# Kernel tuning notes

Hardware: AMD Instinct MI355X
Metric: run time of the kernel (lower is better)

## Reference

```python
import jax, jax.numpy as jnp
import numpy as np

B = 1_000_000  # number of tracklets
STATE_DIM, OBS_DIM = 6, 3


def setup_inputs() -> dict:
    key = jax.random.key(0)
    k1, k2, k3, k4 = jax.random.split(key, 4)
    x = jax.random.normal(k1, (B, STATE_DIM, 1), dtype=jnp.float32)
    # P: symmetric PSD covariance, eye + small random A A^T
    A = 0.1 * jax.random.normal(k2, (B, STATE_DIM, STATE_DIM), dtype=jnp.float32)
    P = jnp.einsum('bij,bkj->bik', A, A) + jnp.eye(STATE_DIM, dtype=jnp.float32)
    delta_t = jax.random.uniform(k3, (B,), dtype=jnp.float32, minval=0.01, maxval=0.2)
    Q = jnp.broadcast_to(0.01 * jnp.eye(STATE_DIM, dtype=jnp.float32), (B, STATE_DIM, STATE_DIM))
    z = jax.random.normal(k4, (B, OBS_DIM, 1), dtype=jnp.float32)
    R = jnp.broadcast_to(0.1 * jnp.eye(OBS_DIM, dtype=jnp.float32), (B, OBS_DIM, OBS_DIM))
    return {"x": x, "P": P, "delta_t": delta_t, "Q": Q, "z": z, "R": R}


def reference(x, P, delta_t, Q, z, R):
    """One batched EKF step: predict(delta_t, Q) then update(z, R).
    Returns (x_upd [B,6,1], P_upd [B,6,6])."""
    Bn = x.shape[0]
    dt = delta_t.reshape(-1)
    # F = I6 with dt on the (pos, vel) off-diagonal entries (0,3),(1,4),(2,5)
    shift = jnp.zeros((STATE_DIM, STATE_DIM), x.dtype).at[
        jnp.array([0, 1, 2]), jnp.array([3, 4, 5])].set(1.0)
    F = jnp.eye(STATE_DIM, dtype=x.dtype) + dt[:, None, None] * shift  # [B,6,6]

    # Predict
    x_pred = F @ x                                           # [B,6,1]
    P_pred = F @ P @ jnp.swapaxes(F, -1, -2) + Q             # [B,6,6]

    # Update (H selects first 3 state rows, so H@P == P[:, :3, :], etc.)
    S = P_pred[:, :OBS_DIM, :OBS_DIM] + R                    # [B,3,3]
    K = P_pred[:, :, :OBS_DIM] @ jnp.linalg.inv(S)           # [B,6,3]
    innov = z - x_pred[:, :OBS_DIM, :]                       # [B,3,1]
    x_upd = x_pred + K @ innov                               # [B,6,1]
    # K @ H places K in the first 3 columns of a [B,6,6] matrix
    KH = jnp.concatenate([K, jnp.zeros((Bn, STATE_DIM, STATE_DIM - OBS_DIM), x.dtype)], axis=2)
    P_upd = P_pred - KH @ P_pred                             # (I - K H) P
    return x_upd, P_upd
```

## Files before the change

### kernel.cpp

```cpp
#include <hip/hip_runtime.h>


#define BLK 256

__global__ __launch_bounds__(BLK, 5)
void ekf_step_r7(const float* __restrict__ x_in,
                 const float* __restrict__ P_in,
                 const float* __restrict__ dt_in,
                 const float* __restrict__ Q_in,
                 const float* __restrict__ z_in,
                 const float* __restrict__ R_in,
                 float* __restrict__ x_out,
                 float* __restrict__ P_out,
                 int B)
{
    const int t = blockIdx.x * BLK + threadIdx.x;
    if (t >= B) return;

    float Qu[36];
#pragma unroll
    for (int j = 0; j < 36; ++j) Qu[j] = Q_in[j];
    float Ru[9];
#pragma unroll
    for (int j = 0; j < 9; ++j) Ru[j] = R_in[j];

    float P[36];
    {
        const float4* pr = (const float4*)(P_in + (size_t)t * 36);
#pragma unroll
        for (int k = 0; k < 9; ++k) {
            float4 v = pr[k];
            P[k*4+0] = v.x; P[k*4+1] = v.y; P[k*4+2] = v.z; P[k*4+3] = v.w;
        }
    }

    const float dt = dt_in[t];

    float x[6];
    {
        const float2* p = (const float2*)(x_in + (size_t)t * 6);
        float2 a = p[0], b = p[1], c = p[2];
        x[0]=a.x; x[1]=a.y; x[2]=b.x; x[3]=b.y; x[4]=c.x; x[5]=c.y;
    }
    float zv[3];
    {
        const float* p = z_in + (size_t)t * 3;
        zv[0]=p[0]; zv[1]=p[1]; zv[2]=p[2];
    }

    float xp[6];
#pragma unroll
    for (int i = 0; i < 3; ++i) xp[i] = fmaf(dt, x[i+3], x[i]);
    xp[3]=x[3]; xp[4]=x[4]; xp[5]=x[5];

#pragma unroll
    for (int i = 0; i < 3; ++i)
#pragma unroll
        for (int j = 0; j < 6; ++j)
            P[i*6+j] = fmaf(dt, P[(i+3)*6+j], P[i*6+j]);
#pragma unroll
    for (int i = 0; i < 6; ++i)
#pragma unroll
        for (int j = 0; j < 3; ++j)
            P[i*6+j] = fmaf(dt, P[i*6+j+3], P[i*6+j]);
#pragma unroll
    for (int j = 0; j < 36; ++j)
        P[j] += Qu[j];

    const float S00 = P[0]  + Ru[0], S01 = P[1]  + Ru[1], S02 = P[2]  + Ru[2];
    const float S10 = P[6]  + Ru[3], S11 = P[7]  + Ru[4], S12 = P[8]  + Ru[5];
    const float S20 = P[12] + Ru[6], S21 = P[13] + Ru[7], S22 = P[14] + Ru[8];

    const float c00 =  (S11*S22 - S12*S21);
    const float c01 = -(S10*S22 - S12*S20);
    const float c02 =  (S10*S21 - S11*S20);
    const float c10 = -(S01*S22 - S02*S21);
    const float c11 =  (S00*S22 - S02*S20);
    const float c12 = -(S00*S21 - S01*S20);
    const float c20 =  (S01*S12 - S02*S11);
    const float c21 = -(S00*S12 - S02*S10);
    const float c22 =  (S00*S11 - S01*S10);
    const float det  = S00*c00 + S01*c01 + S02*c02;
    const float rdet = 1.0f / det;

    float Si[9];
    Si[0]=c00*rdet; Si[1]=c10*rdet; Si[2]=c20*rdet;
    Si[3]=c01*rdet; Si[4]=c11*rdet; Si[5]=c21*rdet;
    Si[6]=c02*rdet; Si[7]=c12*rdet; Si[8]=c22*rdet;

    float K[18];
#pragma unroll
    for (int i = 0; i < 6; ++i)
#pragma unroll
        for (int a = 0; a < 3; ++a)
            K[i*3+a] = P[i*6+0]*Si[0*3+a] + P[i*6+1]*Si[1*3+a] + P[i*6+2]*Si[2*3+a];

    const float iv0 = zv[0] - xp[0];
    const float iv1 = zv[1] - xp[1];
    const float iv2 = zv[2] - xp[2];

    float xu[6];
#pragma unroll
    for (int i = 0; i < 6; ++i)
        xu[i] = xp[i] + K[i*3+0]*iv0 + K[i*3+1]*iv1 + K[i*3+2]*iv2;

    {
        float2* p = (float2*)(x_out + (size_t)t * 6);
        p[0] = make_float2(xu[0], xu[1]);
        p[1] = make_float2(xu[2], xu[3]);
        p[2] = make_float2(xu[4], xu[5]);
    }

    float T[18];
#pragma unroll
    for (int j = 0; j < 18; ++j) T[j] = P[j];
#pragma unroll
    for (int i = 0; i < 6; ++i)
#pragma unroll
        for (int j = 0; j < 6; ++j)
            P[i*6+j] -= K[i*3+0]*T[j] + K[i*3+1]*T[6+j] + K[i*3+2]*T[12+j];

    {
        float4* gq = (float4*)(P_out + (size_t)t * 36);
#pragma unroll
        for (int k = 0; k < 9; ++k)
            gq[k] = make_float4(P[k*4+0], P[k*4+1], P[k*4+2], P[k*4+3]);
    }
}

extern "C" void kernel_launch(void* const* d_in, const int* in_sizes, int n_in,
                              void* d_out, int out_size, void* d_ws, size_t ws_size,
                              hipStream_t stream) {
    const float* x_in  = (const float*)d_in[0];
    const float* P_in  = (const float*)d_in[1];
    const float* dt_in = (const float*)d_in[2];
    const float* Q_in  = (const float*)d_in[3];
    const float* z_in  = (const float*)d_in[4];
    const float* R_in  = (const float*)d_in[5];

    const int B = in_sizes[2];

    float* x_out = (float*)d_out;
    float* P_out = (float*)d_out + (size_t)B * 6;

    const int grid = (B + BLK - 1) / BLK;
    ekf_step_r7<<<grid, BLK, 0, stream>>>(x_in, P_in, dt_in, Q_in, z_in, R_in,
                                          x_out, P_out, B);
}
```

Before: 382.9 us.

## Use persistent grid-stride loop with double-buffered register prefetch and nontemporal stores

Replaces the one-thread-per-tracklet launch with a capped grid of 1024 blocks that loops over tracklets. Each thread prefetches the next tracklet's P, x, z and dt into a second register buffer while it computes the current one, so memory latency overlaps with math. Outputs are written with nontemporal stores, and the occupancy hint drops from 5 to 4 blocks per SIMD. The second buffer raises register pressure and cuts occupancy, and the capped grid may leave the memory pipes less saturated than a full launch would.

Measured after the change: 668.4 us. +74.6%, slower.

```diff
diff --git a/kernel.cpp b/kernel.cpp
--- a/kernel.cpp
+++ b/kernel.cpp
@@ -2,56 +2,65 @@
 
 
 #define BLK 256
-
-__global__ __launch_bounds__(BLK, 5)
-void ekf_step_r7(const float* __restrict__ x_in,
-                 const float* __restrict__ P_in,
-                 const float* __restrict__ dt_in,
-                 const float* __restrict__ Q_in,
-                 const float* __restrict__ z_in,
-                 const float* __restrict__ R_in,
-                 float* __restrict__ x_out,
-                 float* __restrict__ P_out,
-                 int B)
+#define MAXG 1024
+
+typedef float vf4 __attribute__((ext_vector_type(4)));
+typedef float vf2 __attribute__((ext_vector_type(2)));
+
+struct Trk {
+    vf4   pv[9];
+    float x0,x1,x2,x3,x4,x5;
+    float z0,z1,z2;
+    float dt;
+};
+
+__device__ __forceinline__ void load_trk(Trk& T, int t, int B,
+                                         const float* __restrict__ P_in,
+                                         const float* __restrict__ x_in,
+                                         const float* __restrict__ z_in,
+                                         const float* __restrict__ dt_in)
 {
-    const int t = blockIdx.x * BLK + threadIdx.x;
-    if (t >= B) return;
-
-    float Qu[36];
-#pragma unroll
-    for (int j = 0; j < 36; ++j) Qu[j] = Q_in[j];
-    float Ru[9];
-#pragma unroll
-    for (int j = 0; j < 9; ++j) Ru[j] = R_in[j];
+    const bool v = (t < B);
+    const vf4* pr = (const vf4*)(P_in + (size_t)t * 36);
+#pragma unroll
+    for (int k = 0; k < 9; ++k) {
+        T.pv[k] = (vf4)(0.f);
+        if (v) T.pv[k] = pr[k];
+    }
+    T.x0=T.x1=T.x2=T.x3=T.x4=T.x5=0.f;
+    if (v) {
+        const vf2* p = (const vf2*)(x_in + (size_t)t * 6);
+        vf2 a = p[0], b = p[1], c = p[2];
+        T.x0=a.x; T.x1=a.y; T.x2=b.x; T.x3=b.y; T.x4=c.x; T.x5=c.y;
+    }
+    T.z0=T.z1=T.z2=0.f;
+    if (v) {
+        const float* p = z_in + (size_t)t * 3;
+        T.z0=p[0]; T.z1=p[1]; T.z2=p[2];
+    }
+    T.dt = 0.f;
+    if (v) T.dt = dt_in[t];
+}
+
+__device__ __forceinline__ void proc_trk(const Trk& T, int t, int B,
+                                         const float* Qu, const float* Ru,
+                                         float* __restrict__ x_out,
+                                         float* __restrict__ P_out)
+{
+    const float dt = T.dt;
 
     float P[36];
-    {
-        const float4* pr = (const float4*)(P_in + (size_t)t * 36);
-#pragma unroll
-        for (int k = 0; k < 9; ++k) {
-            float4 v = pr[k];
-            P[k*4+0] = v.x; P[k*4+1] = v.y; P[k*4+2] = v.z; P[k*4+3] = v.w;
-        }
-    }
-
-    const float dt = dt_in[t];
-
-    float x[6];
-    {
-        const float2* p = (const float2*)(x_in + (size_t)t * 6);
-        float2 a = p[0], b = p[1], c = p[2];
-        x[0]=a.x; x[1]=a.y; x[2]=b.x; x[3]=b.y; x[4]=c.x; x[5]=c.y;
-    }
-    float zv[3];
-    {
-        const float* p = z_in + (size_t)t * 3;
-        zv[0]=p[0]; zv[1]=p[1]; zv[2]=p[2];
+#pragma unroll
+    for (int k = 0; k < 9; ++k) {
+        P[k*4+0]=T.pv[k].x; P[k*4+1]=T.pv[k].y;
+        P[k*4+2]=T.pv[k].z; P[k*4+3]=T.pv[k].w;
     }
 
     float xp[6];
-#pragma unroll
-    for (int i = 0; i < 3; ++i) xp[i] = fmaf(dt, x[i+3], x[i]);
-    xp[3]=x[3]; xp[4]=x[4]; xp[5]=x[5];
+    xp[0] = fmaf(dt, T.x3, T.x0);
+    xp[1] = fmaf(dt, T.x4, T.x1);
+    xp[2] = fmaf(dt, T.x5, T.x2);
+    xp[3] = T.x3; xp[4] = T.x4; xp[5] = T.x5;
 
 #pragma unroll
     for (int i = 0; i < 3; ++i)
@@ -95,36 +104,78 @@
         for (int a = 0; a < 3; ++a)
             K[i*3+a] = P[i*6+0]*Si[0*3+a] + P[i*6+1]*Si[1*3+a] + P[i*6+2]*Si[2*3+a];
 
-    const float iv0 = zv[0] - xp[0];
-    const float iv1 = zv[1] - xp[1];
-    const float iv2 = zv[2] - xp[2];
-
-    float xu[6];
-#pragma unroll
-    for (int i = 0; i < 6; ++i)
-        xu[i] = xp[i] + K[i*3+0]*iv0 + K[i*3+1]*iv1 + K[i*3+2]*iv2;
-
-    {
-        float2* p = (float2*)(x_out + (size_t)t * 6);
-        p[0] = make_float2(xu[0], xu[1]);
-        p[1] = make_float2(xu[2], xu[3]);
-        p[2] = make_float2(xu[4], xu[5]);
-    }
-
-    float T[18];
-#pragma unroll
-    for (int j = 0; j < 18; ++j) T[j] = P[j];
-#pragma unroll
-    for (int i = 0; i < 6; ++i)
-#pragma unroll
-        for (int j = 0; j < 6; ++j)
-            P[i*6+j] -= K[i*3+0]*T[j] + K[i*3+1]*T[6+j] + K[i*3+2]*T[12+j];
-
-    {
-        float4* gq = (float4*)(P_out + (size_t)t * 36);
-#pragma unroll
-        for (int k = 0; k < 9; ++k)
-            gq[k] = make_float4(P[k*4+0], P[k*4+1], P[k*4+2], P[k*4+3]);
+    const float iv0 = T.z0 - xp[0];
+    const float iv1 = T.z1 - xp[1];
+    const float iv2 = T.z2 - xp[2];
+
+    const bool v = (t < B);
+    if (v) {
+        vf2* p = (vf2*)(x_out + (size_t)t * 6);
+        vf2 r0 = {xp[0] + K[0]*iv0  + K[1]*iv1  + K[2]*iv2,
+                  xp[1] + K[3]*iv0  + K[4]*iv1  + K[5]*iv2};
+        vf2 r1 = {xp[2] + K[6]*iv0  + K[7]*iv1  + K[8]*iv2,
+                  xp[3] + K[9]*iv0  + K[10]*iv1 + K[11]*iv2};
+        vf2 r2 = {xp[4] + K[12]*iv0 + K[13]*iv1 + K[14]*iv2,
+                  xp[5] + K[15]*iv0 + K[16]*iv1 + K[17]*iv2};
+        __builtin_nontemporal_store(r0, p + 0);
+        __builtin_nontemporal_store(r1, p + 1);
+        __builtin_nontemporal_store(r2, p + 2);
+    }
+
+#pragma unroll
+    for (int j = 0; j < 6; ++j) {
+        const float p0 = P[j], p1 = P[6+j], p2 = P[12+j];
+#pragma unroll
+        for (int i = 0; i < 6; ++i)
+            P[i*6+j] -= K[i*3+0]*p0 + K[i*3+1]*p1 + K[i*3+2]*p2;
+    }
+
+    if (v) {
+        vf4* gq = (vf4*)(P_out + (size_t)t * 36);
+#pragma unroll
+        for (int k = 0; k < 9; ++k) {
+            vf4 w = {P[k*4+0], P[k*4+1], P[k*4+2], P[k*4+3]};
+            __builtin_nontemporal_store(w, gq + k);
+        }
+    }
+}
+
+__global__ __launch_bounds__(BLK, 4)
+void ekf_step_r10(const float* __restrict__ x_in,
+                  const float* __restrict__ P_in,
+                  const float* __restrict__ dt_in,
+                  const float* __restrict__ Q_in,
+                  const float* __restrict__ z_in,
+                  const float* __restrict__ R_in,
+                  float* __restrict__ x_out,
+                  float* __restrict__ P_out,
+                  int B)
+{
+    const int tid0   = blockIdx.x * BLK + threadIdx.x;
+    const int stride = gridDim.x * BLK;
+    const int niter  = (B + stride - 1) / stride;
+
+    float Qu[36];
+#pragma unroll
+    for (int j = 0; j < 36; ++j) Qu[j] = Q_in[j];
+    float Ru[9];
+#pragma unroll
+    for (int j = 0; j < 9; ++j) Ru[j] = R_in[j];
+
+    Trk A, Bb;
+    load_trk(A, tid0, B, P_in, x_in, z_in, dt_in);
+
+    int k = 0;
+    while (true) {
+        if (k + 1 < niter)
+            load_trk(Bb, tid0 + (k+1)*stride, B, P_in, x_in, z_in, dt_in);
+        proc_trk(A, tid0 + k*stride, B, Qu, Ru, x_out, P_out);
+        ++k; if (k == niter) break;
+
+        if (k + 1 < niter)
+            load_trk(A, tid0 + (k+1)*stride, B, P_in, x_in, z_in, dt_in);
+        proc_trk(Bb, tid0 + k*stride, B, Qu, Ru, x_out, P_out);
+        ++k; if (k == niter) break;
     }
 }
 
@@ -143,7 +194,8 @@
     float* x_out = (float*)d_out;
     float* P_out = (float*)d_out + (size_t)B * 6;
 
-    const int grid = (B + BLK - 1) / BLK;
-    ekf_step_r7<<<grid, BLK, 0, stream>>>(x_in, P_in, dt_in, Q_in, z_in, R_in,
-                                          x_out, P_out, B);
-}
+    int grid = (B + BLK - 1) / BLK;
+    if (grid > MAXG) grid = MAXG;
+    ekf_step_r10<<<grid, BLK, 0, stream>>>(x_in, P_in, dt_in, Q_in, z_in, R_in,
+                                           x_out, P_out, B);
+}
```

## Stage inputs through LDS with async global_load_lds triple-buffered persistent pipeline

Applied to the files above, without the earlier changes.

Replaces the one-thread-per-tracklet kernel with a persistent grid of 64-thread blocks. Each block walks 64-element tiles and stages P, x, z and dt into a three-slot LDS ring using direct global-to-LDS loads, overlapping the loads for later tiles with compute on the current one through vmcnt waits. Outputs use nontemporal stores. This aims to get coalesced, deeply pipelined memory traffic for a bandwidth-bound kernel, but the grid is capped at 1024 blocks of 64 threads, which limits occupancy and depends on hand-counted vmcnt values being correct.

After: 652.4 us. 70.4% more time.

```diff
diff --git a/kernel.cpp b/kernel.cpp
--- a/kernel.cpp
+++ b/kernel.cpp
@@ -1,57 +1,92 @@
 #include <hip/hip_runtime.h>
 
 
-#define BLK 256
-
-__global__ __launch_bounds__(BLK, 5)
-void ekf_step_r7(const float* __restrict__ x_in,
-                 const float* __restrict__ P_in,
-                 const float* __restrict__ dt_in,
-                 const float* __restrict__ Q_in,
-                 const float* __restrict__ z_in,
-                 const float* __restrict__ R_in,
-                 float* __restrict__ x_out,
-                 float* __restrict__ P_out,
-                 int B)
+#define BLK   64
+#define TFL   2944
+#define XOFF  2304
+#define ZOFF  2688
+#define DOFF  2880
+#define MAXG  1024
+
+typedef float vf4 __attribute__((ext_vector_type(4)));
+typedef float vf2 __attribute__((ext_vector_type(2)));
+
+__device__ __forceinline__ void gl16(const float* g, float* l) {
+    __builtin_amdgcn_global_load_lds(
+        (const __attribute__((address_space(1))) void*)g,
+        (__attribute__((address_space(3))) void*)l, 16, 0, 0);
+}
+__device__ __forceinline__ void gl4(const float* g, float* l) {
+    __builtin_amdgcn_global_load_lds(
+        (const __attribute__((address_space(1))) void*)g,
+        (__attribute__((address_space(3))) void*)l, 4, 0, 0);
+}
+
+#define VMWAIT(N) do { \
+    asm volatile("s_waitcnt vmcnt(" #N ")" ::: "memory"); \
+    __builtin_amdgcn_sched_barrier(0); \
+} while (0)
+
+__device__ __forceinline__ void stage_tile(float* buf, int tt, int lane,
+    const float* __restrict__ P_in, const float* __restrict__ x_in,
+    const float* __restrict__ z_in, const float* __restrict__ dt_in,
+    int pmax, int xmax, int zmax, int dmax)
 {
-    const int t = blockIdx.x * BLK + threadIdx.x;
-    if (t >= B) return;
-
-    float Qu[36];
-#pragma unroll
-    for (int j = 0; j < 36; ++j) Qu[j] = Q_in[j];
-    float Ru[9];
-#pragma unroll
-    for (int j = 0; j < 9; ++j) Ru[j] = R_in[j];
+#pragma unroll
+    for (int op = 0; op < 9; ++op) {
+        int e = tt*2304 + op*256 + lane*4;
+        e = min(e, pmax);
+        gl16(P_in + e, buf + op*256);
+    }
+#pragma unroll
+    for (int op = 0; op < 6; ++op) {
+        int e = tt*384 + op*64 + lane;
+        e = min(e, xmax);
+        gl4(x_in + e, buf + XOFF + op*64);
+    }
+#pragma unroll
+    for (int op = 0; op < 3; ++op) {
+        int e = tt*192 + op*64 + lane;
+        e = min(e, zmax);
+        gl4(z_in + e, buf + ZOFF + op*64);
+    }
+    {
+        int e = tt*64 + lane;
+        e = min(e, dmax);
+        gl4(dt_in + e, buf + DOFF);
+    }
+}
+
+__device__ __forceinline__ void proc_tile(const float* buf, int tt, int lane,
+    int B, const float* Qu, const float* Ru,
+    float* __restrict__ x_out, float* __restrict__ P_out)
+{
+    const int t = tt*64 + lane;
+    const bool valid = (t < B);
 
     float P[36];
-    {
-        const float4* pr = (const float4*)(P_in + (size_t)t * 36);
-#pragma unroll
-        for (int k = 0; k < 9; ++k) {
-            float4 v = pr[k];
-            P[k*4+0] = v.x; P[k*4+1] = v.y; P[k*4+2] = v.z; P[k*4+3] = v.w;
-        }
-    }
-
-    const float dt = dt_in[t];
-
+#pragma unroll
+    for (int q = 0; q < 9; ++q) {
+        vf4 v = *(const vf4*)(buf + 36*lane + 4*q);
+        P[4*q+0]=v.x; P[4*q+1]=v.y; P[4*q+2]=v.z; P[4*q+3]=v.w;
+    }
     float x[6];
     {
-        const float2* p = (const float2*)(x_in + (size_t)t * 6);
-        float2 a = p[0], b = p[1], c = p[2];
+        vf2 a = *(const vf2*)(buf + XOFF + 6*lane + 0);
+        vf2 b = *(const vf2*)(buf + XOFF + 6*lane + 2);
+        vf2 c = *(const vf2*)(buf + XOFF + 6*lane + 4);
         x[0]=a.x; x[1]=a.y; x[2]=b.x; x[3]=b.y; x[4]=c.x; x[5]=c.y;
     }
-    float zv[3];
-    {
-        const float* p = z_in + (size_t)t * 3;
-        zv[0]=p[0]; zv[1]=p[1]; zv[2]=p[2];
-    }
+    const float zv0 = buf[ZOFF + 3*lane + 0];
+    const float zv1 = buf[ZOFF + 3*lane + 1];
+    const float zv2 = buf[ZOFF + 3*lane + 2];
+    const float dt  = buf[DOFF + lane];
 
     float xp[6];
-#pragma unroll
-    for (int i = 0; i < 3; ++i) xp[i] = fmaf(dt, x[i+3], x[i]);
-    xp[3]=x[3]; xp[4]=x[4]; xp[5]=x[5];
+    xp[0] = fmaf(dt, x[3], x[0]);
+    xp[1] = fmaf(dt, x[4], x[1]);
+    xp[2] = fmaf(dt, x[5], x[2]);
+    xp[3] = x[3]; xp[4] = x[4]; xp[5] = x[5];
 
 #pragma unroll
     for (int i = 0; i < 3; ++i)
@@ -95,37 +130,98 @@
         for (int a = 0; a < 3; ++a)
             K[i*3+a] = P[i*6+0]*Si[0*3+a] + P[i*6+1]*Si[1*3+a] + P[i*6+2]*Si[2*3+a];
 
-    const float iv0 = zv[0] - xp[0];
-    const float iv1 = zv[1] - xp[1];
-    const float iv2 = zv[2] - xp[2];
-
-    float xu[6];
-#pragma unroll
-    for (int i = 0; i < 6; ++i)
-        xu[i] = xp[i] + K[i*3+0]*iv0 + K[i*3+1]*iv1 + K[i*3+2]*iv2;
-
-    {
-        float2* p = (float2*)(x_out + (size_t)t * 6);
-        p[0] = make_float2(xu[0], xu[1]);
-        p[1] = make_float2(xu[2], xu[3]);
-        p[2] = make_float2(xu[4], xu[5]);
-    }
-
-    float T[18];
-#pragma unroll
-    for (int j = 0; j < 18; ++j) T[j] = P[j];
-#pragma unroll
-    for (int i = 0; i < 6; ++i)
-#pragma unroll
-        for (int j = 0; j < 6; ++j)
-            P[i*6+j] -= K[i*3+0]*T[j] + K[i*3+1]*T[6+j] + K[i*3+2]*T[12+j];
-
-    {
-        float4* gq = (float4*)(P_out + (size_t)t * 36);
-#pragma unroll
-        for (int k = 0; k < 9; ++k)
-            gq[k] = make_float4(P[k*4+0], P[k*4+1], P[k*4+2], P[k*4+3]);
-    }
+    const float iv0 = zv0 - xp[0];
+    const float iv1 = zv1 - xp[1];
+    const float iv2 = zv2 - xp[2];
+
+    if (valid) {
+        vf2* p = (vf2*)(x_out + (size_t)t * 6);
+        vf2 r0 = {xp[0] + K[0]*iv0  + K[1]*iv1  + K[2]*iv2,
+                  xp[1] + K[3]*iv0  + K[4]*iv1  + K[5]*iv2};
+        vf2 r1 = {xp[2] + K[6]*iv0  + K[7]*iv1  + K[8]*iv2,
+                  xp[3] + K[9]*iv0  + K[10]*iv1 + K[11]*iv2};
+        vf2 r2 = {xp[4] + K[12]*iv0 + K[13]*iv1 + K[14]*iv2,
+                  xp[5] + K[15]*iv0 + K[16]*iv1 + K[17]*iv2};
+        __builtin_nontemporal_store(r0, p + 0);
+        __builtin_nontemporal_store(r1, p + 1);
+        __builtin_nontemporal_store(r2, p + 2);
+    }
+
+#pragma unroll
+    for (int j = 0; j < 6; ++j) {
+        const float p0 = P[j], p1 = P[6+j], p2 = P[12+j];
+#pragma unroll
+        for (int i = 0; i < 6; ++i)
+            P[i*6+j] -= K[i*3+0]*p0 + K[i*3+1]*p1 + K[i*3+2]*p2;
+    }
+
+    if (valid) {
+        vf4* gq = (vf4*)(P_out + (size_t)t * 36);
+#pragma unroll
+        for (int k = 0; k < 9; ++k) {
+            vf4 w = {P[k*4+0], P[k*4+1], P[k*4+2], P[k*4+3]};
+            __builtin_nontemporal_store(w, gq + k);
+        }
+    }
+}
+
+__global__ __launch_bounds__(BLK, 2)
+void ekf_r11(const float* __restrict__ x_in,
+             const float* __restrict__ P_in,
+             const float* __restrict__ dt_in,
+             const float* __restrict__ Q_in,
+             const float* __restrict__ z_in,
+             const float* __restrict__ R_in,
+             float* __restrict__ x_out,
+             float* __restrict__ P_out,
+             int B)
+{
+    __shared__ float sm[3 * TFL];
+    const int lane   = threadIdx.x;
+    const int g      = gridDim.x;
+    const int bb     = blockIdx.x;
+    const int ntiles = (B + 63) >> 6;
+    const int nt     = (ntiles - bb + g - 1) / g;
+    if (nt <= 0) return;
+
+    const int pmax = B*36 - 4, xmax = B*6 - 1, zmax = B*3 - 1, dmax = B - 1;
+
+    float Qu[36], Ru[9];
+#pragma unroll
+    for (int j = 0; j < 36; ++j) Qu[j] = Q_in[j];
+#pragma unroll
+    for (int j = 0; j < 9; ++j) Ru[j] = R_in[j];
+
+#define STG(RING, K) stage_tile(sm + (RING)*TFL, bb + (K)*g, lane, \
+                                P_in, x_in, z_in, dt_in, pmax, xmax, zmax, dmax)
+#define PRC(RING, K) proc_tile(sm + (RING)*TFL, bb + (K)*g, lane, B, Qu, Ru, \
+                               x_out, P_out)
+
+    if (nt >= 5) {
+        STG(0, 0);
+        STG(1, 1);
+        STG(2, 2); VMWAIT(38); PRC(0, 0);
+        STG(0, 3); VMWAIT(48); PRC(1, 1);
+        for (int k = 2; k <= nt - 3; ++k) {
+            const int rs = (k + 2) % 3, r = k % 3;
+            stage_tile(sm + rs*TFL, bb + (k+2)*g, lane,
+                       P_in, x_in, z_in, dt_in, pmax, xmax, zmax, dmax);
+            VMWAIT(58);
+            proc_tile(sm + r*TFL, bb + k*g, lane, B, Qu, Ru, x_out, P_out);
+        }
+        VMWAIT(39); PRC((nt - 2) % 3, nt - 2);
+        VMWAIT(20); PRC((nt - 1) % 3, nt - 1);
+    } else {
+        for (int k = 0; k < nt; ++k) {
+            const int r = k % 3;
+            stage_tile(sm + r*TFL, bb + k*g, lane,
+                       P_in, x_in, z_in, dt_in, pmax, xmax, zmax, dmax);
+            VMWAIT(0);
+            proc_tile(sm + r*TFL, bb + k*g, lane, B, Qu, Ru, x_out, P_out);
+        }
+    }
+#undef STG
+#undef PRC
 }
 
 extern "C" void kernel_launch(void* const* d_in, const int* in_sizes, int n_in,
@@ -143,7 +239,9 @@
     float* x_out = (float*)d_out;
     float* P_out = (float*)d_out + (size_t)B * 6;
 
-    const int grid = (B + BLK - 1) / BLK;
-    ekf_step_r7<<<grid, BLK, 0, stream>>>(x_in, P_in, dt_in, Q_in, z_in, R_in,
-                                          x_out, P_out, B);
-}
+    int ntiles = (B + 63) >> 6;
+    int grid = ntiles < MAXG ? ntiles : MAXG;
+    if (grid < 1) grid = 1;
+    ekf_r11<<<grid, BLK, 0, stream>>>(x_in, P_in, dt_in, Q_in, z_in, R_in,
+                                      x_out, P_out, B);
+}
```
